# Kernel optimization log

Hardware: AMD Instinct MI355X
Metric: run time of the kernel (lower is better)

## Reference

```python
import jax, jax.numpy as jnp
import numpy as np

B, T, C, H, O = 256, 256, 32, 512, 32
OUT_TIME = 32


def setup_inputs() -> dict:
    key = jax.random.key(0)
    ks = jax.random.split(key, 10)
    times = jnp.arange(T, dtype=jnp.float32)
    coeffs = jax.random.normal(ks[0], (B, T, C), jnp.float32)
    final_index = jax.random.randint(ks[1], (B,), 0, T)
    dW = jax.random.normal(ks[2], (T - 1, B, H), jnp.float32)  # unit-normal; scaled by sqrt(dt) inside
    s = lambda k, shape, fan: jax.random.normal(k, shape, jnp.float32) / np.float32(np.sqrt(fan))
    return {
        "times": times, "coeffs": coeffs, "final_index": final_index, "dW": dW,
        "W_init": s(ks[3], (C, H), C), "b_init": jnp.zeros((H,), jnp.float32),
        "W1": s(ks[4], (H + C, H), H + C), "b1": jnp.zeros((H,), jnp.float32),
        "W2": s(ks[5], (H, H), H), "b2": jnp.zeros((H,), jnp.float32),
        "Wg": s(ks[6], (H, H), H), "bg": jnp.zeros((H,), jnp.float32),
        "Wh1": s(ks[7], (H, H), H), "bh1": jnp.zeros((H,), jnp.float32),
        "Wh2": s(ks[8], (H, O), H), "bh2": jnp.zeros((O,), jnp.float32),
    }


def reference(times, coeffs, final_index, dW, W_init, b_init, W1, b1, W2, b2, Wg, bg, Wh1, bh1, Wh2, bh2):
    # dt = max(min(diff(times)), 0.001)  (Euler method default in the torch module)
    dt = jnp.maximum(jnp.min(times[1:] - times[:-1]), jnp.float32(0.001))
    sqdt = jnp.sqrt(dt)

    x_seq = jnp.transpose(coeffs, (1, 0, 2))  # [T, B, C] control path at grid points
    # z0 = initial_network(X.evaluate(times[0]))
    z0 = x_seq[0] @ W_init + b_init  # [B, H]

    def step(y, inp):
        xk, dWk = inp  # [B, C], [B, H]
        h = jnp.tanh(jnp.concatenate([y, xk], axis=-1) @ W1 + b1)
        f = jnp.tanh(h @ W2 + b2)                # drift
        g = jax.nn.sigmoid(y @ Wg + bg)          # diagonal diffusion
        y_next = y + f * dt + g * (sqdt * dWk)   # Euler-Maruyama step
        return y_next, y_next

    _, zs = jax.lax.scan(step, z0, (x_seq[:-1], dW))  # zs: [T-1, B, H]
    z = jnp.concatenate([z0[None], zs], axis=0)       # [T, B, H]
    z = jnp.transpose(z, (1, 0, 2))                   # [B, T, H]  (transpose loop in torch code)
    z_tail = z[:, z.shape[1] - OUT_TIME:, :]          # last output_time steps
    return jax.nn.relu(z_tail @ Wh1 + bh1) @ Wh2 + bh2  # [B, OUT_TIME, O]
```

## Files before the change

### kernel.cpp

```cpp
#include <hip/hip_runtime.h>
#include <stdint.h>
#include <stddef.h>

typedef __attribute__((ext_vector_type(8))) short short8;
typedef __attribute__((ext_vector_type(8))) _Float16 half8;
typedef __attribute__((ext_vector_type(4))) float f32x4;
typedef unsigned long long ull;

#define T_  256
#define B_  256
#define C_  32
#define H_  512
#define O_  32
#define KB1 17
#define NT1 64
#define KB2 16
#define NT2 32

__device__ __forceinline__ short f2h(float f) {
  _Float16 h = (_Float16)f;
  return __builtin_bit_cast(short, h);
}
__device__ __forceinline__ void f2hl(float f, short& hi, short& lo) {
  _Float16 h = (_Float16)f;
  _Float16 l = (_Float16)(f - (float)h);
  hi = __builtin_bit_cast(short, h);
  lo = __builtin_bit_cast(short, l);
}
__device__ __forceinline__ unsigned int pack_hl(float f) {
  short h, l;
  f2hl(f, h, l);
  return (unsigned int)(unsigned short)h | ((unsigned int)(unsigned short)l << 16);
}
__device__ __forceinline__ float fast_tanh(float x) {
  float e = __expf(2.0f * x);
  return 1.0f - 2.0f / (e + 1.0f);
}
__device__ __forceinline__ float fast_sigmoid(float x) {
  return 1.0f / (1.0f + __expf(-x));
}
__device__ __forceinline__ f32x4 mfma16(half8 a, half8 b, f32x4 c) {
  return __builtin_amdgcn_mfma_f32_16x16x32_f16(a, b, c, 0, 0, 0);
}
__device__ __forceinline__ half8 ld8(const short* p) { return *(const half8*)p; }

__device__ __forceinline__ void st_coh(unsigned int* p, unsigned int v) {
  __hip_atomic_store(p, v, __ATOMIC_RELAXED, __HIP_MEMORY_SCOPE_AGENT);
}
__device__ __forceinline__ ull ld_coh(const ull* p) {
  return __hip_atomic_load(p, __ATOMIC_RELAXED, __HIP_MEMORY_SCOPE_AGENT);
}

__device__ __forceinline__ void stage_pl(const ull* src, short* hi, short* lo,
                                         int stride, int tid) {
  ull v[16];
  #pragma unroll
  for (int i = 0; i < 8; ++i) {
    int p = i * 256 + tid;
    v[2 * i]     = ld_coh(src + 2 * p);
    v[2 * i + 1] = ld_coh(src + 2 * p + 1);
  }
  #pragma unroll
  for (int i = 0; i < 8; ++i) {
    int p = i * 256 + tid;
    int row = p >> 7, col4 = (p & 127) << 2;
    unsigned int u0 = (unsigned int)v[2 * i],     u1 = (unsigned int)(v[2 * i] >> 32);
    unsigned int u2 = (unsigned int)v[2 * i + 1], u3 = (unsigned int)(v[2 * i + 1] >> 32);
    unsigned int hiA = (u0 & 0xffffu) | (u1 << 16);
    unsigned int hiB = (u2 & 0xffffu) | (u3 << 16);
    unsigned int loA = (u0 >> 16) | (u1 & 0xffff0000u);
    unsigned int loB = (u2 >> 16) | (u3 & 0xffff0000u);
    *(ull*)(hi + row * stride + col4) = (ull)hiA | ((ull)hiB << 32);
    *(ull*)(lo + row * stride + col4) = (ull)loA | ((ull)loB << 32);
  }
}

__device__ __forceinline__ void bg_barrier(unsigned int* cnt, unsigned int target) {
  __syncthreads();
  if (threadIdx.x == 0) {
    __hip_atomic_fetch_add(cnt, 1u, __ATOMIC_RELAXED, __HIP_MEMORY_SCOPE_AGENT);
    while (__hip_atomic_load(cnt, __ATOMIC_RELAXED, __HIP_MEMORY_SCOPE_AGENT) < target)
      __builtin_amdgcn_s_sleep(1);
  }
  __syncthreads();
}

__global__ void pack_b1s(const float* __restrict__ W1, const float* __restrict__ Wg,
                         short* __restrict__ hi, short* __restrict__ lo) {
  int gid = blockIdx.x * 256 + threadIdx.x;
  if (gid >= KB1 * NT1 * 512) return;
  int j = gid & 7, lane = (gid >> 3) & 63, tile = gid >> 9;
  int nt = tile % NT1, kb = tile / NT1;
  int k = kb * 32 + ((lane >> 4) << 3) + j;
  int n = ((nt & 31) << 4) + (lane & 15);
  float v = 0.f;
  if (nt < 32)      v = W1[k * H_ + n];
  else if (k < H_)  v = Wg[k * H_ + n];
  short h, l;
  f2hl(v, h, l);
  hi[gid] = h; lo[gid] = l;
}

__global__ void pack_s(const float* __restrict__ src, short* __restrict__ hi,
                       short* __restrict__ lo, int Ksrc, int Nsrc, int KB, int NT) {
  int gid = blockIdx.x * 256 + threadIdx.x;
  if (gid >= KB * NT * 512) return;
  int j = gid & 7, lane = (gid >> 3) & 63, tile = gid >> 9;
  int nt = tile % NT, kb = tile / NT;
  int k = kb * 32 + ((lane >> 4) << 3) + j;
  int n = (nt << 4) + (lane & 15);
  float v = (k < Ksrc && n < Nsrc) ? src[k * Nsrc + n] : 0.f;
  short h, l;
  f2hl(v, h, l);
  hi[gid] = h;
  if (lo) lo[gid] = l;
}

__global__ __launch_bounds__(256, 1) void sde_kernel(
    const float* __restrict__ times, const float* __restrict__ coeffs,
    const float* __restrict__ dW,
    const float* __restrict__ b_init, const float* __restrict__ b1,
    const float* __restrict__ b2, const float* __restrict__ bgb,
    const short* __restrict__ B1h, const short* __restrict__ B1l,
    const short* __restrict__ W2h, const short* __restrict__ W2l,
    const short* __restrict__ WIh, const short* __restrict__ WIl,
    unsigned int* __restrict__ y_pk, unsigned int* __restrict__ h_pk,
    short* __restrict__ zt, unsigned int* __restrict__ cnt_base) {
  __shared__ short yx_hi[16][552];
  __shared__ short yx_lo[16][552];
  __shared__ short hh_hi[16][520];
  __shared__ short hh_lo[16][520];
  __shared__ float g_x[16][32];
  __shared__ float redbuf[4];

  const int tid = threadIdx.x;
  const int w = tid >> 6, l = tid & 63;
  const int ra = l & 15, kq = l >> 4;
  const int bid = blockIdx.x;
  const int bg = bid & 15, cg = bid >> 4;
  const int R0 = bg << 4;
  unsigned int* cnt = cnt_base + bg * 32;

  const int nt1w = (w < 2) ? (2 * cg + w) : (32 + 2 * cg + (w - 2));
  const int extcol = nt1w * 16 + ra;
  const int ntF = 2 * cg + (w & 1);
  const int fcol = ntF * 16 + ra;

  float d = 1e30f;
  if (tid < T_ - 1) d = times[tid + 1] - times[tid];
  #pragma unroll
  for (int s = 32; s >= 1; s >>= 1) d = fminf(d, __shfl_xor(d, s, 64));
  if (l == 0) redbuf[w] = d;

  half8 wb1h[17], wb1l[17];
  #pragma unroll
  for (int kb = 0; kb < 17; ++kb) {
    const size_t off = ((size_t)(kb * 64 + nt1w) << 9) + (l << 3);
    wb1h[kb] = ld8(B1h + off);
    wb1l[kb] = ld8(B1l + off);
  }
  half8 ww2h[16], ww2l[16];
  if (w < 2) {
    #pragma unroll
    for (int kb = 0; kb < 16; ++kb) {
      const size_t off = ((size_t)(kb * 32 + ntF) << 9) + (l << 3);
      ww2h[kb] = ld8(W2h + off);
      ww2l[kb] = ld8(W2l + off);
    }
  }

  if (tid < 64) {
    int row = tid >> 2, cc = (tid & 3) << 3;
    const float* xb = coeffs + (size_t)(R0 + row) * (T_ * C_) + cc;
    short8 hi, lo;
    #pragma unroll
    for (int j = 0; j < 8; ++j) {
      short h, l2;
      f2hl(xb[j], h, l2);
      hi[j] = h; lo[j] = l2;
    }
    *(short8*)&yx_hi[row][512 + cc] = hi;
    *(short8*)&yx_lo[row][512 + cc] = lo;
  }
  __syncthreads();
  float m = fminf(fminf(redbuf[0], redbuf[1]), fminf(redbuf[2], redbuf[3]));
  const float dt = fmaxf(m, 0.001f);
  const float sq = sqrtf(dt);

  const float b1v = (w < 2) ? b1[extcol] : 0.f;
  const float bgv = (w >= 2) ? bgb[extcol - 512] : 0.f;
  const float b2v = (w < 2) ? b2[fcol] : 0.f;

  float yr[4] = {0.f, 0.f, 0.f, 0.f};
  if (w < 2) {
    half8 ah = ld8(&yx_hi[ra][512 + (kq << 3)]);
    half8 al = ld8(&yx_lo[ra][512 + (kq << 3)]);
    half8 bh = ld8(WIh + ((size_t)ntF << 9) + (l << 3));
    half8 bl = ld8(WIl + ((size_t)ntF << 9) + (l << 3));
    f32x4 Z = {0.f, 0.f, 0.f, 0.f};
    Z = mfma16(ah, bh, Z); Z = mfma16(al, bh, Z); Z = mfma16(ah, bl, Z);
    float bi = b_init[fcol];
    #pragma unroll
    for (int r = 0; r < 4; ++r) {
      yr[r] = Z[r] + bi;
      st_coh(&y_pk[(size_t)(R0 + (kq << 2) + r) * H_ + fcol], pack_hl(yr[r]));
    }
  }
  bg_barrier(cnt, 16u);

  for (int k = 0; k < T_ - 1; ++k) {
    float dwv[4];
    if (w < 2) {
      const float* dwb = dW + ((size_t)k * B_ + R0) * H_ + fcol;
      #pragma unroll
      for (int r = 0; r < 4; ++r)
        dwv[r] = __builtin_nontemporal_load(dwb + ((kq << 2) + r) * H_);
    }
    stage_pl((const ull*)y_pk + R0 * 256, &yx_hi[0][0], &yx_lo[0][0], 552, tid);
    __syncthreads();
    f32x4 Aa = {0.f, 0.f, 0.f, 0.f}, Ab = Aa, Ac = Aa;
    #pragma unroll
    for (int kb = 0; kb < 17; ++kb) {
      half8 ah = ld8(&yx_hi[ra][(kb << 5) + (kq << 3)]);
      half8 al = ld8(&yx_lo[ra][(kb << 5) + (kq << 3)]);
      Aa = mfma16(ah, wb1h[kb], Aa);
      Ab = mfma16(al, wb1h[kb], Ab);
      Ac = mfma16(ah, wb1l[kb], Ac);
    }
    if (w < 2) {
      #pragma unroll
      for (int r = 0; r < 4; ++r) {
        float h = fast_tanh((Aa[r] + Ab[r]) + Ac[r] + b1v);
        st_coh(&h_pk[(size_t)(R0 + (kq << 2) + r) * H_ + extcol], pack_hl(h));
      }
    } else {
      #pragma unroll
      for (int r = 0; r < 4; ++r)
        g_x[(kq << 2) + r][((w - 2) << 4) + ra] =
            fast_sigmoid((Aa[r] + Ab[r]) + Ac[r] + bgv);
    }
    bg_barrier(cnt, 16u * (2u * (unsigned)k + 2u));
    stage_pl((const ull*)h_pk + R0 * 256, &hh_hi[0][0], &hh_lo[0][0], 520, tid);
    __syncthreads();
    if (w < 2) {
      f32x4 Fa = {0.f, 0.f, 0.f, 0.f}, Fb = Fa, Fc = Fa;
      #pragma unroll
      for (int kb = 0; kb < 16; ++kb) {
        half8 ah = ld8(&hh_hi[ra][(kb << 5) + (kq << 3)]);
        half8 al = ld8(&hh_lo[ra][(kb << 5) + (kq << 3)]);
        Fa = mfma16(ah, ww2h[kb], Fa);
        Fb = mfma16(al, ww2h[kb], Fb);
        Fc = mfma16(ah, ww2l[kb], Fc);
      }
      #pragma unroll
      for (int r = 0; r < 4; ++r) {
        float f = fast_tanh((Fa[r] + Fb[r]) + Fc[r] + b2v);
        float g = g_x[(kq << 2) + r][((w & 1) << 4) + ra];
        yr[r] += f * dt + g * (sq * dwv[r]);
        st_coh(&y_pk[(size_t)(R0 + (kq << 2) + r) * H_ + fcol], pack_hl(yr[r]));
      }
      if (k >= T_ - 1 - O_) {
        int t = k - (T_ - 1 - O_);
        #pragma unroll
        for (int r = 0; r < 4; ++r)
          zt[((size_t)(R0 + (kq << 2) + r) * O_ + t) * H_ + fcol] = f2h(yr[r]);
      }
    } else if (w == 2 && k < T_ - 2) {
      int row = l >> 2, cc = (l & 3) << 3;
      const float* xb =
          coeffs + (size_t)(R0 + row) * (T_ * C_) + (size_t)(k + 1) * C_ + cc;
      short8 hi, lo;
      #pragma unroll
      for (int j = 0; j < 8; ++j) {
        short h, l2;
        f2hl(xb[j], h, l2);
        hi[j] = h; lo[j] = l2;
      }
      *(short8*)&yx_hi[row][512 + cc] = hi;
      *(short8*)&yx_lo[row][512 + cc] = lo;
    }
    bg_barrier(cnt, 16u * (2u * (unsigned)k + 3u));
  }
}

__global__ __launch_bounds__(256) void head_kernel(
    const short* __restrict__ zt, const short* __restrict__ Wh1p,
    const short* __restrict__ Wh2p, const float* __restrict__ bh1,
    const float* __restrict__ bh2, float* __restrict__ out) {
  __shared__ short a_lds[32][520];
  __shared__ short h2_lds[32][520];
  const int tid = threadIdx.x;
  const int w = tid >> 6, l = tid & 63;
  const int ra = l & 15, kq = l >> 4;
  const int r0 = blockIdx.x << 5;

  const short* zb = zt + (size_t)r0 * H_;
  #pragma unroll
  for (int i = 0; i < 8; ++i) {
    int cidx = i * 256 + tid;
    int row = cidx >> 6, cc = (cidx & 63) << 3;
    *(short8*)&a_lds[row][cc] = *(const short8*)(zb + row * H_ + cc);
  }
  __syncthreads();

  f32x4 acc[2][8];
  #pragma unroll
  for (int mt = 0; mt < 2; ++mt)
    #pragma unroll
    for (int i = 0; i < 8; ++i) acc[mt][i] = (f32x4){0.f, 0.f, 0.f, 0.f};
  for (int kb = 0; kb < 16; ++kb) {
    half8 a0 = ld8(&a_lds[ra][(kb << 5) + (kq << 3)]);
    half8 a1 = ld8(&a_lds[16 + ra][(kb << 5) + (kq << 3)]);
    const short* bp = Wh1p + (size_t)kb * (32 * 512) + (l << 3);
    #pragma unroll
    for (int i = 0; i < 8; ++i) {
      half8 b = ld8(bp + ((8 * w + i) << 9));
      acc[0][i] = mfma16(a0, b, acc[0][i]);
      acc[1][i] = mfma16(a1, b, acc[1][i]);
    }
  }
  #pragma unroll
  for (int i = 0; i < 8; ++i) {
    int col = ((8 * w + i) << 4) + ra;
    float bb = bh1[col];
    #pragma unroll
    for (int mt = 0; mt < 2; ++mt)
      #pragma unroll
      for (int r = 0; r < 4; ++r) {
        float h = acc[mt][i][r] + bb;
        h = h > 0.f ? h : 0.f;
        h2_lds[(mt << 4) + (kq << 2) + r][col] = f2h(h);
      }
  }
  __syncthreads();

  {
    int mt = w >> 1, nt = w & 1;
    f32x4 F = {0.f, 0.f, 0.f, 0.f};
    for (int kb = 0; kb < 16; ++kb) {
      half8 a = ld8(&h2_lds[(mt << 4) + ra][(kb << 5) + (kq << 3)]);
      half8 b = ld8(Wh2p + (size_t)((kb * 2 + nt) * 64 + l) * 8);
      F = mfma16(a, b, F);
    }
    int col = (nt << 4) + ra;
    float bb = bh2[col];
    #pragma unroll
    for (int r = 0; r < 4; ++r)
      out[(size_t)(r0 + (mt << 4) + (kq << 2) + r) * O_ + col] = F[r] + bb;
  }
}

extern "C" void kernel_launch(void* const* d_in, const int* in_sizes, int n_in,
                              void* d_out, int out_size, void* d_ws, size_t ws_size,
                              hipStream_t stream) {
  (void)in_sizes; (void)n_in; (void)out_size; (void)ws_size;
  const float* times  = (const float*)d_in[0];
  const float* coeffs = (const float*)d_in[1];
  const float* dW     = (const float*)d_in[3];
  const float* W_init = (const float*)d_in[4];
  const float* b_init = (const float*)d_in[5];
  const float* W1     = (const float*)d_in[6];
  const float* b1     = (const float*)d_in[7];
  const float* W2     = (const float*)d_in[8];
  const float* b2     = (const float*)d_in[9];
  const float* Wg     = (const float*)d_in[10];
  const float* bg     = (const float*)d_in[11];
  const float* Wh1    = (const float*)d_in[12];
  const float* bh1    = (const float*)d_in[13];
  const float* Wh2    = (const float*)d_in[14];
  const float* bh2    = (const float*)d_in[15];
  float* out = (float*)d_out;
  char* ws = (char*)d_ws;

  short* B1h  = (short*)(ws + 0);
  short* B1l  = (short*)(ws + 1114112);
  short* W2h  = (short*)(ws + 2228224);
  short* W2l  = (short*)(ws + 2752512);
  short* WIh  = (short*)(ws + 3276800);
  short* WIl  = (short*)(ws + 3309568);
  short* Wh1p = (short*)(ws + 3342336);
  short* Wh2p = (short*)(ws + 3866624);
  unsigned int* y_pk = (unsigned int*)(ws + 3899392);
  unsigned int* h_pk = (unsigned int*)(ws + 4423680);
  short* zt   = (short*)(ws + 4947968);
  unsigned int* cnt = (unsigned int*)(ws + 13336576);

  pack_b1s<<<2176, 256, 0, stream>>>(W1, Wg, B1h, B1l);
  pack_s  <<<1024, 256, 0, stream>>>(W2, W2h, W2l, 512, 512, 16, 32);
  pack_s  <<<64,   256, 0, stream>>>(W_init, WIh, WIl, 32, 512, 1, 32);
  pack_s  <<<1024, 256, 0, stream>>>(Wh1, Wh1p, (short*)nullptr, 512, 512, 16, 32);
  pack_s  <<<64,   256, 0, stream>>>(Wh2, Wh2p, (short*)nullptr, 512, 32, 16, 2);

  hipMemsetAsync(ws + 13336576, 0, 2048, stream);

  sde_kernel<<<256, 256, 0, stream>>>(times, coeffs, dW, b_init, b1, b2, bg,
                                      B1h, B1l, W2h, W2l, WIh, WIl,
                                      y_pk, h_pk, zt, cnt);
  head_kernel<<<256, 256, 0, stream>>>(zt, Wh1p, Wh2p, bh1, bh2, out);
}
```

Before: 1.511 ms.

## Use 512-thread blocks and per-block flag barriers in the SDE loop

Halves the grid to 128 blocks of 512 threads, so each block computes four column tiles instead of two and each batch group has 8 cooperating blocks instead of 16. The shared atomic-counter barrier becomes per-block monotonic flags: each block publishes its step counter, and every wave polls the group's eight flags before staging shared state. This is meant to cut inter-block synchronisation latency and atomic contention on each of the two per-step barriers. In exchange, launch_bounds(512,2) tightens the per-thread register budget while the kernel keeps large register-resident weight fragments, which risks spilling.

Measured after the change: 2.839 ms. 87.9% more time.

```diff
diff --git a/kernel.cpp b/kernel.cpp
--- a/kernel.cpp
+++ b/kernel.cpp
@@ -47,22 +47,25 @@
 __device__ __forceinline__ void st_coh(unsigned int* p, unsigned int v) {
   __hip_atomic_store(p, v, __ATOMIC_RELAXED, __HIP_MEMORY_SCOPE_AGENT);
 }
+__device__ __forceinline__ unsigned int ld_cohu(const unsigned int* p) {
+  return __hip_atomic_load(p, __ATOMIC_RELAXED, __HIP_MEMORY_SCOPE_AGENT);
+}
 __device__ __forceinline__ ull ld_coh(const ull* p) {
   return __hip_atomic_load(p, __ATOMIC_RELAXED, __HIP_MEMORY_SCOPE_AGENT);
 }
 
 __device__ __forceinline__ void stage_pl(const ull* src, short* hi, short* lo,
                                          int stride, int tid) {
-  ull v[16];
-  #pragma unroll
-  for (int i = 0; i < 8; ++i) {
-    int p = i * 256 + tid;
+  ull v[8];
+  #pragma unroll
+  for (int i = 0; i < 4; ++i) {
+    int p = i * 512 + tid;
     v[2 * i]     = ld_coh(src + 2 * p);
     v[2 * i + 1] = ld_coh(src + 2 * p + 1);
   }
   #pragma unroll
-  for (int i = 0; i < 8; ++i) {
-    int p = i * 256 + tid;
+  for (int i = 0; i < 4; ++i) {
+    int p = i * 512 + tid;
     int row = p >> 7, col4 = (p & 127) << 2;
     unsigned int u0 = (unsigned int)v[2 * i],     u1 = (unsigned int)(v[2 * i] >> 32);
     unsigned int u2 = (unsigned int)v[2 * i + 1], u3 = (unsigned int)(v[2 * i + 1] >> 32);
@@ -75,14 +78,13 @@
   }
 }
 
-__device__ __forceinline__ void bg_barrier(unsigned int* cnt, unsigned int target) {
-  __syncthreads();
-  if (threadIdx.x == 0) {
-    __hip_atomic_fetch_add(cnt, 1u, __ATOMIC_RELAXED, __HIP_MEMORY_SCOPE_AGENT);
-    while (__hip_atomic_load(cnt, __ATOMIC_RELAXED, __HIP_MEMORY_SCOPE_AGENT) < target)
-      __builtin_amdgcn_s_sleep(1);
-  }
-  __syncthreads();
+__device__ __forceinline__ void bg_wait(const unsigned int* fl, unsigned int target) {
+  const int l = threadIdx.x & 63;
+  for (;;) {
+    unsigned int f = (l < 8) ? ld_cohu(fl + l * 32) : 0xffffffffu;
+    if (__all((l < 8) ? (f >= target) : 1)) break;
+  }
+  __builtin_amdgcn_sched_barrier(0);
 }
 
 __global__ void pack_b1s(const float* __restrict__ W1, const float* __restrict__ Wg,
@@ -116,7 +118,7 @@
   if (lo) lo[gid] = l;
 }
 
-__global__ __launch_bounds__(256, 1) void sde_kernel(
+__global__ __launch_bounds__(512, 2) void sde_kernel(
     const float* __restrict__ times, const float* __restrict__ coeffs,
     const float* __restrict__ dW,
     const float* __restrict__ b_init, const float* __restrict__ b1,
@@ -125,12 +127,12 @@
     const short* __restrict__ W2h, const short* __restrict__ W2l,
     const short* __restrict__ WIh, const short* __restrict__ WIl,
     unsigned int* __restrict__ y_pk, unsigned int* __restrict__ h_pk,
-    short* __restrict__ zt, unsigned int* __restrict__ cnt_base) {
+    short* __restrict__ zt, unsigned int* __restrict__ flags_base) {
   __shared__ short yx_hi[16][552];
   __shared__ short yx_lo[16][552];
   __shared__ short hh_hi[16][520];
   __shared__ short hh_lo[16][520];
-  __shared__ float g_x[16][32];
+  __shared__ float g_x[16][64];
   __shared__ float redbuf[4];
 
   const int tid = threadIdx.x;
@@ -139,18 +141,19 @@
   const int bid = blockIdx.x;
   const int bg = bid & 15, cg = bid >> 4;
   const int R0 = bg << 4;
-  unsigned int* cnt = cnt_base + bg * 32;
-
-  const int nt1w = (w < 2) ? (2 * cg + w) : (32 + 2 * cg + (w - 2));
+  unsigned int* flags = flags_base + (bg << 3) * 32;
+  unsigned int* myflag = flags + cg * 32;
+
+  const int nt1w = (w < 4) ? (4 * cg + w) : (32 + 4 * cg + (w - 4));
   const int extcol = nt1w * 16 + ra;
-  const int ntF = 2 * cg + (w & 1);
+  const int ntF = 4 * cg + (w & 3);
   const int fcol = ntF * 16 + ra;
 
   float d = 1e30f;
   if (tid < T_ - 1) d = times[tid + 1] - times[tid];
   #pragma unroll
   for (int s = 32; s >= 1; s >>= 1) d = fminf(d, __shfl_xor(d, s, 64));
-  if (l == 0) redbuf[w] = d;
+  if (w < 4 && l == 0) redbuf[w] = d;
 
   half8 wb1h[17], wb1l[17];
   #pragma unroll
@@ -160,7 +163,7 @@
     wb1l[kb] = ld8(B1l + off);
   }
   half8 ww2h[16], ww2l[16];
-  if (w < 2) {
+  if (w < 4) {
     #pragma unroll
     for (int kb = 0; kb < 16; ++kb) {
       const size_t off = ((size_t)(kb * 32 + ntF) << 9) + (l << 3);
@@ -187,12 +190,12 @@
   const float dt = fmaxf(m, 0.001f);
   const float sq = sqrtf(dt);
 
-  const float b1v = (w < 2) ? b1[extcol] : 0.f;
-  const float bgv = (w >= 2) ? bgb[extcol - 512] : 0.f;
-  const float b2v = (w < 2) ? b2[fcol] : 0.f;
+  const float b1v = (w < 4) ? b1[extcol] : 0.f;
+  const float bgv = (w >= 4) ? bgb[extcol - 512] : 0.f;
+  const float b2v = (w < 4) ? b2[fcol] : 0.f;
 
   float yr[4] = {0.f, 0.f, 0.f, 0.f};
-  if (w < 2) {
+  if (w < 4) {
     half8 ah = ld8(&yx_hi[ra][512 + (kq << 3)]);
     half8 al = ld8(&yx_lo[ra][512 + (kq << 3)]);
     half8 bh = ld8(WIh + ((size_t)ntF << 9) + (l << 3));
@@ -206,16 +209,18 @@
       st_coh(&y_pk[(size_t)(R0 + (kq << 2) + r) * H_ + fcol], pack_hl(yr[r]));
     }
   }
-  bg_barrier(cnt, 16u);
+  __syncthreads();
+  if (tid == 0) st_coh(myflag, 1u);
 
   for (int k = 0; k < T_ - 1; ++k) {
     float dwv[4];
-    if (w < 2) {
+    if (w < 4) {
       const float* dwb = dW + ((size_t)k * B_ + R0) * H_ + fcol;
       #pragma unroll
       for (int r = 0; r < 4; ++r)
         dwv[r] = __builtin_nontemporal_load(dwb + ((kq << 2) + r) * H_);
     }
+    bg_wait(flags, 2u * (unsigned)k + 1u);
     stage_pl((const ull*)y_pk + R0 * 256, &yx_hi[0][0], &yx_lo[0][0], 552, tid);
     __syncthreads();
     f32x4 Aa = {0.f, 0.f, 0.f, 0.f}, Ab = Aa, Ac = Aa;
@@ -227,7 +232,7 @@
       Ab = mfma16(al, wb1h[kb], Ab);
       Ac = mfma16(ah, wb1l[kb], Ac);
     }
-    if (w < 2) {
+    if (w < 4) {
       #pragma unroll
       for (int r = 0; r < 4; ++r) {
         float h = fast_tanh((Aa[r] + Ab[r]) + Ac[r] + b1v);
@@ -236,13 +241,16 @@
     } else {
       #pragma unroll
       for (int r = 0; r < 4; ++r)
-        g_x[(kq << 2) + r][((w - 2) << 4) + ra] =
+        g_x[(kq << 2) + r][((w - 4) << 4) + ra] =
             fast_sigmoid((Aa[r] + Ab[r]) + Ac[r] + bgv);
     }
-    bg_barrier(cnt, 16u * (2u * (unsigned)k + 2u));
+    __syncthreads();
+    if (tid == 0) st_coh(myflag, 2u * (unsigned)k + 2u);
+
+    bg_wait(flags, 2u * (unsigned)k + 2u);
     stage_pl((const ull*)h_pk + R0 * 256, &hh_hi[0][0], &hh_lo[0][0], 520, tid);
     __syncthreads();
-    if (w < 2) {
+    if (w < 4) {
       f32x4 Fa = {0.f, 0.f, 0.f, 0.f}, Fb = Fa, Fc = Fa;
       #pragma unroll
       for (int kb = 0; kb < 16; ++kb) {
@@ -255,7 +263,7 @@
       #pragma unroll
       for (int r = 0; r < 4; ++r) {
         float f = fast_tanh((Fa[r] + Fb[r]) + Fc[r] + b2v);
-        float g = g_x[(kq << 2) + r][((w & 1) << 4) + ra];
+        float g = g_x[(kq << 2) + r][((w & 3) << 4) + ra];
         yr[r] += f * dt + g * (sq * dwv[r]);
         st_coh(&y_pk[(size_t)(R0 + (kq << 2) + r) * H_ + fcol], pack_hl(yr[r]));
       }
@@ -265,7 +273,7 @@
         for (int r = 0; r < 4; ++r)
           zt[((size_t)(R0 + (kq << 2) + r) * O_ + t) * H_ + fcol] = f2h(yr[r]);
       }
-    } else if (w == 2 && k < T_ - 2) {
+    } else if (w == 4 && k < T_ - 2) {
       int row = l >> 2, cc = (l & 3) << 3;
       const float* xb =
           coeffs + (size_t)(R0 + row) * (T_ * C_) + (size_t)(k + 1) * C_ + cc;
@@ -279,7 +287,8 @@
       *(short8*)&yx_hi[row][512 + cc] = hi;
       *(short8*)&yx_lo[row][512 + cc] = lo;
     }
-    bg_barrier(cnt, 16u * (2u * (unsigned)k + 3u));
+    __syncthreads();
+    if (tid == 0) st_coh(myflag, 2u * (unsigned)k + 3u);
   }
 }
 
@@ -383,7 +392,7 @@
   unsigned int* y_pk = (unsigned int*)(ws + 3899392);
   unsigned int* h_pk = (unsigned int*)(ws + 4423680);
   short* zt   = (short*)(ws + 4947968);
-  unsigned int* cnt = (unsigned int*)(ws + 13336576);
+  unsigned int* flags = (unsigned int*)(ws + 13336576);
 
   pack_b1s<<<2176, 256, 0, stream>>>(W1, Wg, B1h, B1l);
   pack_s  <<<1024, 256, 0, stream>>>(W2, W2h, W2l, 512, 512, 16, 32);
@@ -391,10 +400,10 @@
   pack_s  <<<1024, 256, 0, stream>>>(Wh1, Wh1p, (short*)nullptr, 512, 512, 16, 32);
   pack_s  <<<64,   256, 0, stream>>>(Wh2, Wh2p, (short*)nullptr, 512, 32, 16, 2);
 
-  hipMemsetAsync(ws + 13336576, 0, 2048, stream);
-
-  sde_kernel<<<256, 256, 0, stream>>>(times, coeffs, dW, b_init, b1, b2, bg,
+  hipMemsetAsync(ws + 13336576, 0, 16384, stream);
+
+  sde_kernel<<<128, 512, 0, stream>>>(times, coeffs, dW, b_init, b1, b2, bg,
                                       B1h, B1l, W2h, W2l, WIh, WIl,
-                                      y_pk, h_pk, zt, cnt);
+                                      y_pk, h_pk, zt, flags);
   head_kernel<<<256, 256, 0, stream>>>(zt, Wh1p, Wh2p, bh1, bh2, out);
 }
```

## Replace atomic counter barrier with per-block flags and split arrive/wait

Applied to the files above, without the earlier changes.

Swaps the shared atomic-increment barrier for per-block monotonic flags. Each block publishes its phase with a relaxed store after a local sync, and waits by having one wavefront poll all 16 peer flags in parallel until every flag reaches the target. This removes atomic contention on one counter and the second __syncthreads, and moves the dW load ahead of the wait so it overlaps. Relaxed atomics without explicit fences carry a memory-ordering risk, and every wavefront now spin-polls without sleeping, which can add memory traffic.

Result: slower. 1.735 ms (+14.8%).

```diff
diff --git a/kernel.cpp b/kernel.cpp
--- a/kernel.cpp
+++ b/kernel.cpp
@@ -46,6 +46,9 @@
 
 __device__ __forceinline__ void st_coh(unsigned int* p, unsigned int v) {
   __hip_atomic_store(p, v, __ATOMIC_RELAXED, __HIP_MEMORY_SCOPE_AGENT);
+}
+__device__ __forceinline__ unsigned int ld_cohu(const unsigned int* p) {
+  return __hip_atomic_load(p, __ATOMIC_RELAXED, __HIP_MEMORY_SCOPE_AGENT);
 }
 __device__ __forceinline__ ull ld_coh(const ull* p) {
   return __hip_atomic_load(p, __ATOMIC_RELAXED, __HIP_MEMORY_SCOPE_AGENT);
@@ -75,14 +78,13 @@
   }
 }
 
-__device__ __forceinline__ void bg_barrier(unsigned int* cnt, unsigned int target) {
-  __syncthreads();
-  if (threadIdx.x == 0) {
-    __hip_atomic_fetch_add(cnt, 1u, __ATOMIC_RELAXED, __HIP_MEMORY_SCOPE_AGENT);
-    while (__hip_atomic_load(cnt, __ATOMIC_RELAXED, __HIP_MEMORY_SCOPE_AGENT) < target)
-      __builtin_amdgcn_s_sleep(1);
-  }
-  __syncthreads();
+__device__ __forceinline__ void bg_wait(const unsigned int* fl, unsigned int target) {
+  const int l = threadIdx.x & 63;
+  for (;;) {
+    unsigned int f = (l < 16) ? ld_cohu(fl + l * 32) : 0xffffffffu;
+    if (__all((l < 16) ? (f >= target) : 1)) break;
+  }
+  __builtin_amdgcn_sched_barrier(0);
 }
 
 __global__ void pack_b1s(const float* __restrict__ W1, const float* __restrict__ Wg,
@@ -125,7 +127,7 @@
     const short* __restrict__ W2h, const short* __restrict__ W2l,
     const short* __restrict__ WIh, const short* __restrict__ WIl,
     unsigned int* __restrict__ y_pk, unsigned int* __restrict__ h_pk,
-    short* __restrict__ zt, unsigned int* __restrict__ cnt_base) {
+    short* __restrict__ zt, unsigned int* __restrict__ flags_base) {
   __shared__ short yx_hi[16][552];
   __shared__ short yx_lo[16][552];
   __shared__ short hh_hi[16][520];
@@ -139,7 +141,8 @@
   const int bid = blockIdx.x;
   const int bg = bid & 15, cg = bid >> 4;
   const int R0 = bg << 4;
-  unsigned int* cnt = cnt_base + bg * 32;
+  unsigned int* flags = flags_base + (bg << 4) * 32;
+  unsigned int* myflag = flags + cg * 32;
 
   const int nt1w = (w < 2) ? (2 * cg + w) : (32 + 2 * cg + (w - 2));
   const int extcol = nt1w * 16 + ra;
@@ -206,7 +209,8 @@
       st_coh(&y_pk[(size_t)(R0 + (kq << 2) + r) * H_ + fcol], pack_hl(yr[r]));
     }
   }
-  bg_barrier(cnt, 16u);
+  __syncthreads();
+  if (tid == 0) st_coh(myflag, 1u);
 
   for (int k = 0; k < T_ - 1; ++k) {
     float dwv[4];
@@ -216,6 +220,7 @@
       for (int r = 0; r < 4; ++r)
         dwv[r] = __builtin_nontemporal_load(dwb + ((kq << 2) + r) * H_);
     }
+    bg_wait(flags, 2u * (unsigned)k + 1u);
     stage_pl((const ull*)y_pk + R0 * 256, &yx_hi[0][0], &yx_lo[0][0], 552, tid);
     __syncthreads();
     f32x4 Aa = {0.f, 0.f, 0.f, 0.f}, Ab = Aa, Ac = Aa;
@@ -239,7 +244,10 @@
         g_x[(kq << 2) + r][((w - 2) << 4) + ra] =
             fast_sigmoid((Aa[r] + Ab[r]) + Ac[r] + bgv);
     }
-    bg_barrier(cnt, 16u * (2u * (unsigned)k + 2u));
+    __syncthreads();
+    if (tid == 0) st_coh(myflag, 2u * (unsigned)k + 2u);
+
+    bg_wait(flags, 2u * (unsigned)k + 2u);
     stage_pl((const ull*)h_pk + R0 * 256, &hh_hi[0][0], &hh_lo[0][0], 520, tid);
     __syncthreads();
     if (w < 2) {
@@ -279,7 +287,8 @@
       *(short8*)&yx_hi[row][512 + cc] = hi;
       *(short8*)&yx_lo[row][512 + cc] = lo;
     }
-    bg_barrier(cnt, 16u * (2u * (unsigned)k + 3u));
+    __syncthreads();
+    if (tid == 0) st_coh(myflag, 2u * (unsigned)k + 3u);
   }
 }
 
@@ -383,7 +392,7 @@
   unsigned int* y_pk = (unsigned int*)(ws + 3899392);
   unsigned int* h_pk = (unsigned int*)(ws + 4423680);
   short* zt   = (short*)(ws + 4947968);
-  unsigned int* cnt = (unsigned int*)(ws + 13336576);
+  unsigned int* flags = (unsigned int*)(ws + 13336576);
 
   pack_b1s<<<2176, 256, 0, stream>>>(W1, Wg, B1h, B1l);
   pack_s  <<<1024, 256, 0, stream>>>(W2, W2h, W2l, 512, 512, 16, 32);
@@ -391,10 +400,10 @@
   pack_s  <<<1024, 256, 0, stream>>>(Wh1, Wh1p, (short*)nullptr, 512, 512, 16, 32);
   pack_s  <<<64,   256, 0, stream>>>(Wh2, Wh2p, (short*)nullptr, 512, 32, 16, 2);
 
-  hipMemsetAsync(ws + 13336576, 0, 2048, stream);
+  hipMemsetAsync(ws + 13336576, 0, 32768, stream);
 
   sde_kernel<<<256, 256, 0, stream>>>(times, coeffs, dW, b_init, b1, b2, bg,
                                       B1h, B1l, W2h, W2l, WIh, WIl,
-                                      y_pk, h_pk, zt, cnt);
+                                      y_pk, h_pk, zt, flags);
   head_kernel<<<256, 256, 0, stream>>>(zt, Wh1p, Wh2p, bh1, bh2, out);
 }
```

## Split each block's batch rows into two independent 8-row groups to overlap barrier waits

Applied to the files above, without the earlier changes.

Each block now serves two independent 8-row batch groups (A and B), each with its own cross-block counter. The blocking barrier is split into separate signal and wait steps, so one group's compute can run while the other group's barrier latency is pending. The cost is that the 16x16 MFMA tiles are only half used (8 valid rows), roughly doubling MFMA issue per useful row, and the group counters need twice the memset space.

Measured after the change: 2.206 ms. 46.0% more time.

```diff
diff --git a/kernel.cpp b/kernel.cpp
--- a/kernel.cpp
+++ b/kernel.cpp
@@ -3,6 +3,7 @@
 #include <stddef.h>
 
 typedef __attribute__((ext_vector_type(8))) short short8;
+typedef __attribute__((ext_vector_type(4))) short short4v;
 typedef __attribute__((ext_vector_type(8))) _Float16 half8;
 typedef __attribute__((ext_vector_type(4))) float f32x4;
 typedef unsigned long long ull;
@@ -51,38 +52,41 @@
   return __hip_atomic_load(p, __ATOMIC_RELAXED, __HIP_MEMORY_SCOPE_AGENT);
 }
 
-__device__ __forceinline__ void stage_pl(const ull* src, short* hi, short* lo,
-                                         int stride, int tid) {
-  ull v[16];
-  #pragma unroll
-  for (int i = 0; i < 8; ++i) {
-    int p = i * 256 + tid;
-    v[2 * i]     = ld_coh(src + 2 * p);
-    v[2 * i + 1] = ld_coh(src + 2 * p + 1);
-  }
-  #pragma unroll
-  for (int i = 0; i < 8; ++i) {
-    int p = i * 256 + tid;
-    int row = p >> 7, col4 = (p & 127) << 2;
+__device__ __forceinline__ void sig(unsigned int* cnt) {
+  __syncthreads();
+  if (threadIdx.x == 0)
+    __hip_atomic_fetch_add(cnt, 1u, __ATOMIC_RELAXED, __HIP_MEMORY_SCOPE_AGENT);
+}
+__device__ __forceinline__ void wt(unsigned int* cnt, unsigned int target) {
+  if (threadIdx.x == 0) {
+    while (__hip_atomic_load(cnt, __ATOMIC_RELAXED, __HIP_MEMORY_SCOPE_AGENT) < target)
+      __builtin_amdgcn_s_sleep(1);
+  }
+  __syncthreads();
+}
+
+__device__ __forceinline__ void stage8(const ull* src, short* hi, short* lo,
+                                       int stride, int tid) {
+  ull v[8];
+  #pragma unroll
+  for (int i = 0; i < 4; ++i) {
+    int u = i * 512 + 2 * tid;
+    v[2 * i]     = ld_coh(src + u);
+    v[2 * i + 1] = ld_coh(src + u + 1);
+  }
+  #pragma unroll
+  for (int i = 0; i < 4; ++i) {
+    int u = i * 512 + 2 * tid;
+    int row = u >> 8, c = (u & 255) * 2;
     unsigned int u0 = (unsigned int)v[2 * i],     u1 = (unsigned int)(v[2 * i] >> 32);
     unsigned int u2 = (unsigned int)v[2 * i + 1], u3 = (unsigned int)(v[2 * i + 1] >> 32);
     unsigned int hiA = (u0 & 0xffffu) | (u1 << 16);
     unsigned int hiB = (u2 & 0xffffu) | (u3 << 16);
     unsigned int loA = (u0 >> 16) | (u1 & 0xffff0000u);
     unsigned int loB = (u2 >> 16) | (u3 & 0xffff0000u);
-    *(ull*)(hi + row * stride + col4) = (ull)hiA | ((ull)hiB << 32);
-    *(ull*)(lo + row * stride + col4) = (ull)loA | ((ull)loB << 32);
-  }
-}
-
-__device__ __forceinline__ void bg_barrier(unsigned int* cnt, unsigned int target) {
-  __syncthreads();
-  if (threadIdx.x == 0) {
-    __hip_atomic_fetch_add(cnt, 1u, __ATOMIC_RELAXED, __HIP_MEMORY_SCOPE_AGENT);
-    while (__hip_atomic_load(cnt, __ATOMIC_RELAXED, __HIP_MEMORY_SCOPE_AGENT) < target)
-      __builtin_amdgcn_s_sleep(1);
-  }
-  __syncthreads();
+    *(ull*)(hi + row * stride + c) = (ull)hiA | ((ull)hiB << 32);
+    *(ull*)(lo + row * stride + c) = (ull)loA | ((ull)loB << 32);
+  }
 }
 
 __global__ void pack_b1s(const float* __restrict__ W1, const float* __restrict__ Wg,
@@ -126,25 +130,27 @@
     const short* __restrict__ WIh, const short* __restrict__ WIl,
     unsigned int* __restrict__ y_pk, unsigned int* __restrict__ h_pk,
     short* __restrict__ zt, unsigned int* __restrict__ cnt_base) {
-  __shared__ short yx_hi[16][552];
-  __shared__ short yx_lo[16][552];
-  __shared__ short hh_hi[16][520];
-  __shared__ short hh_lo[16][520];
-  __shared__ float g_x[16][32];
+  __shared__ short yxA_hi[8][552], yxA_lo[8][552];
+  __shared__ short yxB_hi[8][552], yxB_lo[8][552];
+  __shared__ short hhA_hi[8][520], hhA_lo[8][520];
+  __shared__ short hhB_hi[8][520], hhB_lo[8][520];
+  __shared__ float gA[8][32], gB[8][32];
   __shared__ float redbuf[4];
 
   const int tid = threadIdx.x;
   const int w = tid >> 6, l = tid & 63;
   const int ra = l & 15, kq = l >> 4;
   const int bid = blockIdx.x;
-  const int bg = bid & 15, cg = bid >> 4;
-  const int R0 = bg << 4;
-  unsigned int* cnt = cnt_base + bg * 32;
+  const int pair = bid & 15, cg = bid >> 4;
+  const int R0A = pair << 3, R0B = (pair + 16) << 3;
+  unsigned int* cntA = cnt_base + pair * 32;
+  unsigned int* cntB = cnt_base + (pair + 16) * 32;
 
   const int nt1w = (w < 2) ? (2 * cg + w) : (32 + 2 * cg + (w - 2));
   const int extcol = nt1w * 16 + ra;
   const int ntF = 2 * cg + (w & 1);
   const int fcol = ntF * 16 + ra;
+  const int ra8 = ra & 7;
 
   float d = 1e30f;
   if (tid < T_ - 1) d = times[tid + 1] - times[tid];
@@ -169,18 +175,24 @@
     }
   }
 
-  if (tid < 64) {
-    int row = tid >> 2, cc = (tid & 3) << 3;
-    const float* xb = coeffs + (size_t)(R0 + row) * (T_ * C_) + cc;
-    short8 hi, lo;
+  if (w == 2 || w == 3) {
+    int row = l >> 3, c0 = (l & 7) << 2;
+    const float* xb =
+        coeffs + (size_t)(((w == 2) ? R0A : R0B) + row) * (T_ * C_) + c0;
+    short4v hi, lo;
     #pragma unroll
-    for (int j = 0; j < 8; ++j) {
+    for (int j = 0; j < 4; ++j) {
       short h, l2;
       f2hl(xb[j], h, l2);
       hi[j] = h; lo[j] = l2;
     }
-    *(short8*)&yx_hi[row][512 + cc] = hi;
-    *(short8*)&yx_lo[row][512 + cc] = lo;
+    if (w == 2) {
+      *(short4v*)&yxA_hi[row][512 + c0] = hi;
+      *(short4v*)&yxA_lo[row][512 + c0] = lo;
+    } else {
+      *(short4v*)&yxB_hi[row][512 + c0] = hi;
+      *(short4v*)&yxB_lo[row][512 + c0] = lo;
+    }
   }
   __syncthreads();
   float m = fminf(fminf(redbuf[0], redbuf[1]), fminf(redbuf[2], redbuf[3]));
@@ -191,95 +203,203 @@
   const float bgv = (w >= 2) ? bgb[extcol - 512] : 0.f;
   const float b2v = (w < 2) ? b2[fcol] : 0.f;
 
-  float yr[4] = {0.f, 0.f, 0.f, 0.f};
+  float yrA[4] = {0.f, 0.f, 0.f, 0.f}, yrB[4] = {0.f, 0.f, 0.f, 0.f};
   if (w < 2) {
-    half8 ah = ld8(&yx_hi[ra][512 + (kq << 3)]);
-    half8 al = ld8(&yx_lo[ra][512 + (kq << 3)]);
     half8 bh = ld8(WIh + ((size_t)ntF << 9) + (l << 3));
     half8 bl = ld8(WIl + ((size_t)ntF << 9) + (l << 3));
-    f32x4 Z = {0.f, 0.f, 0.f, 0.f};
-    Z = mfma16(ah, bh, Z); Z = mfma16(al, bh, Z); Z = mfma16(ah, bl, Z);
     float bi = b_init[fcol];
-    #pragma unroll
-    for (int r = 0; r < 4; ++r) {
-      yr[r] = Z[r] + bi;
-      st_coh(&y_pk[(size_t)(R0 + (kq << 2) + r) * H_ + fcol], pack_hl(yr[r]));
-    }
-  }
-  bg_barrier(cnt, 16u);
+    {
+      half8 ah = ld8(&yxA_hi[ra8][512 + (kq << 3)]);
+      half8 al = ld8(&yxA_lo[ra8][512 + (kq << 3)]);
+      f32x4 Z = {0.f, 0.f, 0.f, 0.f};
+      Z = mfma16(ah, bh, Z); Z = mfma16(al, bh, Z); Z = mfma16(ah, bl, Z);
+      if (kq < 2) {
+        #pragma unroll
+        for (int r = 0; r < 4; ++r) {
+          yrA[r] = Z[r] + bi;
+          st_coh(&y_pk[(size_t)(R0A + (kq << 2) + r) * H_ + fcol], pack_hl(yrA[r]));
+        }
+      }
+    }
+    {
+      half8 ah = ld8(&yxB_hi[ra8][512 + (kq << 3)]);
+      half8 al = ld8(&yxB_lo[ra8][512 + (kq << 3)]);
+      f32x4 Z = {0.f, 0.f, 0.f, 0.f};
+      Z = mfma16(ah, bh, Z); Z = mfma16(al, bh, Z); Z = mfma16(ah, bl, Z);
+      if (kq < 2) {
+        #pragma unroll
+        for (int r = 0; r < 4; ++r) {
+          yrB[r] = Z[r] + bi;
+          st_coh(&y_pk[(size_t)(R0B + (kq << 2) + r) * H_ + fcol], pack_hl(yrB[r]));
+        }
+      }
+    }
+  }
+  __syncthreads();
+  if (tid == 0) {
+    __hip_atomic_fetch_add(cntA, 1u, __ATOMIC_RELAXED, __HIP_MEMORY_SCOPE_AGENT);
+    __hip_atomic_fetch_add(cntB, 1u, __ATOMIC_RELAXED, __HIP_MEMORY_SCOPE_AGENT);
+  }
 
   for (int k = 0; k < T_ - 1; ++k) {
-    float dwv[4];
-    if (w < 2) {
-      const float* dwb = dW + ((size_t)k * B_ + R0) * H_ + fcol;
-      #pragma unroll
-      for (int r = 0; r < 4; ++r)
-        dwv[r] = __builtin_nontemporal_load(dwb + ((kq << 2) + r) * H_);
-    }
-    stage_pl((const ull*)y_pk + R0 * 256, &yx_hi[0][0], &yx_lo[0][0], 552, tid);
+    float dwA[4], dwB[4];
+    if (w < 2 && kq < 2) {
+      const float* dwbA = dW + ((size_t)k * B_ + R0A) * H_ + fcol;
+      const float* dwbB = dW + ((size_t)k * B_ + R0B) * H_ + fcol;
+      #pragma unroll
+      for (int r = 0; r < 4; ++r) {
+        dwA[r] = __builtin_nontemporal_load(dwbA + ((kq << 2) + r) * H_);
+        dwB[r] = __builtin_nontemporal_load(dwbB + ((kq << 2) + r) * H_);
+      }
+    }
+
+    wt(cntA, 16u * (2u * (unsigned)k + 1u));
+    stage8((const ull*)y_pk + R0A * 256, &yxA_hi[0][0], &yxA_lo[0][0], 552, tid);
     __syncthreads();
-    f32x4 Aa = {0.f, 0.f, 0.f, 0.f}, Ab = Aa, Ac = Aa;
-    #pragma unroll
-    for (int kb = 0; kb < 17; ++kb) {
-      half8 ah = ld8(&yx_hi[ra][(kb << 5) + (kq << 3)]);
-      half8 al = ld8(&yx_lo[ra][(kb << 5) + (kq << 3)]);
-      Aa = mfma16(ah, wb1h[kb], Aa);
-      Ab = mfma16(al, wb1h[kb], Ab);
-      Ac = mfma16(ah, wb1l[kb], Ac);
-    }
-    if (w < 2) {
-      #pragma unroll
-      for (int r = 0; r < 4; ++r) {
-        float h = fast_tanh((Aa[r] + Ab[r]) + Ac[r] + b1v);
-        st_coh(&h_pk[(size_t)(R0 + (kq << 2) + r) * H_ + extcol], pack_hl(h));
-      }
-    } else {
-      #pragma unroll
-      for (int r = 0; r < 4; ++r)
-        g_x[(kq << 2) + r][((w - 2) << 4) + ra] =
-            fast_sigmoid((Aa[r] + Ab[r]) + Ac[r] + bgv);
-    }
-    bg_barrier(cnt, 16u * (2u * (unsigned)k + 2u));
-    stage_pl((const ull*)h_pk + R0 * 256, &hh_hi[0][0], &hh_lo[0][0], 520, tid);
+    {
+      f32x4 Aa = {0.f, 0.f, 0.f, 0.f}, Ab = Aa, Ac = Aa;
+      #pragma unroll
+      for (int kb = 0; kb < 17; ++kb) {
+        half8 ah = ld8(&yxA_hi[ra8][(kb << 5) + (kq << 3)]);
+        half8 al = ld8(&yxA_lo[ra8][(kb << 5) + (kq << 3)]);
+        Aa = mfma16(ah, wb1h[kb], Aa);
+        Ab = mfma16(al, wb1h[kb], Ab);
+        Ac = mfma16(ah, wb1l[kb], Ac);
+      }
+      if (kq < 2) {
+        if (w < 2) {
+          #pragma unroll
+          for (int r = 0; r < 4; ++r) {
+            float h = fast_tanh((Aa[r] + Ab[r]) + Ac[r] + b1v);
+            st_coh(&h_pk[(size_t)(R0A + (kq << 2) + r) * H_ + extcol], pack_hl(h));
+          }
+        } else {
+          #pragma unroll
+          for (int r = 0; r < 4; ++r)
+            gA[(kq << 2) + r][((w - 2) << 4) + ra] =
+                fast_sigmoid((Aa[r] + Ab[r]) + Ac[r] + bgv);
+        }
+      }
+    }
+    sig(cntA);
+
+    wt(cntB, 16u * (2u * (unsigned)k + 1u));
+    stage8((const ull*)y_pk + R0B * 256, &yxB_hi[0][0], &yxB_lo[0][0], 552, tid);
+    __syncthreads();
+    {
+      f32x4 Aa = {0.f, 0.f, 0.f, 0.f}, Ab = Aa, Ac = Aa;
+      #pragma unroll
+      for (int kb = 0; kb < 17; ++kb) {
+        half8 ah = ld8(&yxB_hi[ra8][(kb << 5) + (kq << 3)]);
+        half8 al = ld8(&yxB_lo[ra8][(kb << 5) + (kq << 3)]);
+        Aa = mfma16(ah, wb1h[kb], Aa);
+        Ab = mfma16(al, wb1h[kb], Ab);
+        Ac = mfma16(ah, wb1l[kb], Ac);
+      }
+      if (kq < 2) {
+        if (w < 2) {
+          #pragma unroll
+          for (int r = 0; r < 4; ++r) {
+            float h = fast_tanh((Aa[r] + Ab[r]) + Ac[r] + b1v);
+            st_coh(&h_pk[(size_t)(R0B + (kq << 2) + r) * H_ + extcol], pack_hl(h));
+          }
+        } else {
+          #pragma unroll
+          for (int r = 0; r < 4; ++r)
+            gB[(kq << 2) + r][((w - 2) << 4) + ra] =
+                fast_sigmoid((Aa[r] + Ab[r]) + Ac[r] + bgv);
+        }
+      }
+    }
+    sig(cntB);
+
+    wt(cntA, 16u * (2u * (unsigned)k + 2u));
+    stage8((const ull*)h_pk + R0A * 256, &hhA_hi[0][0], &hhA_lo[0][0], 520, tid);
     __syncthreads();
     if (w < 2) {
       f32x4 Fa = {0.f, 0.f, 0.f, 0.f}, Fb = Fa, Fc = Fa;
       #pragma unroll
       for (int kb = 0; kb < 16; ++kb) {
-        half8 ah = ld8(&hh_hi[ra][(kb << 5) + (kq << 3)]);
-        half8 al = ld8(&hh_lo[ra][(kb << 5) + (kq << 3)]);
+        half8 ah = ld8(&hhA_hi[ra8][(kb << 5) + (kq << 3)]);
+        half8 al = ld8(&hhA_lo[ra8][(kb << 5) + (kq << 3)]);
         Fa = mfma16(ah, ww2h[kb], Fa);
         Fb = mfma16(al, ww2h[kb], Fb);
         Fc = mfma16(ah, ww2l[kb], Fc);
       }
-      #pragma unroll
-      for (int r = 0; r < 4; ++r) {
-        float f = fast_tanh((Fa[r] + Fb[r]) + Fc[r] + b2v);
-        float g = g_x[(kq << 2) + r][((w & 1) << 4) + ra];
-        yr[r] += f * dt + g * (sq * dwv[r]);
-        st_coh(&y_pk[(size_t)(R0 + (kq << 2) + r) * H_ + fcol], pack_hl(yr[r]));
-      }
-      if (k >= T_ - 1 - O_) {
-        int t = k - (T_ - 1 - O_);
+      if (kq < 2) {
         #pragma unroll
-        for (int r = 0; r < 4; ++r)
-          zt[((size_t)(R0 + (kq << 2) + r) * O_ + t) * H_ + fcol] = f2h(yr[r]);
+        for (int r = 0; r < 4; ++r) {
+          float f = fast_tanh((Fa[r] + Fb[r]) + Fc[r] + b2v);
+          float g = gA[(kq << 2) + r][((w & 1) << 4) + ra];
+          yrA[r] += f * dt + g * (sq * dwA[r]);
+          st_coh(&y_pk[(size_t)(R0A + (kq << 2) + r) * H_ + fcol], pack_hl(yrA[r]));
+        }
+        if (k >= T_ - 1 - O_) {
+          int t = k - (T_ - 1 - O_);
+          #pragma unroll
+          for (int r = 0; r < 4; ++r)
+            zt[((size_t)(R0A + (kq << 2) + r) * O_ + t) * H_ + fcol] = f2h(yrA[r]);
+        }
       }
     } else if (w == 2 && k < T_ - 2) {
-      int row = l >> 2, cc = (l & 3) << 3;
+      int row = l >> 3, c0 = (l & 7) << 2;
       const float* xb =
-          coeffs + (size_t)(R0 + row) * (T_ * C_) + (size_t)(k + 1) * C_ + cc;
-      short8 hi, lo;
-      #pragma unroll
-      for (int j = 0; j < 8; ++j) {
+          coeffs + (size_t)(R0A + row) * (T_ * C_) + (size_t)(k + 1) * C_ + c0;
+      short4v hi, lo;
+      #pragma unroll
+      for (int j = 0; j < 4; ++j) {
         short h, l2;
         f2hl(xb[j], h, l2);
         hi[j] = h; lo[j] = l2;
       }
-      *(short8*)&yx_hi[row][512 + cc] = hi;
-      *(short8*)&yx_lo[row][512 + cc] = lo;
-    }
-    bg_barrier(cnt, 16u * (2u * (unsigned)k + 3u));
+      *(short4v*)&yxA_hi[row][512 + c0] = hi;
+      *(short4v*)&yxA_lo[row][512 + c0] = lo;
+    }
+    sig(cntA);
+
+    wt(cntB, 16u * (2u * (unsigned)k + 2u));
+    stage8((const ull*)h_pk + R0B * 256, &hhB_hi[0][0], &hhB_lo[0][0], 520, tid);
+    __syncthreads();
+    if (w < 2) {
+      f32x4 Fa = {0.f, 0.f, 0.f, 0.f}, Fb = Fa, Fc = Fa;
+      #pragma unroll
+      for (int kb = 0; kb < 16; ++kb) {
+        half8 ah = ld8(&hhB_hi[ra8][(kb << 5) + (kq << 3)]);
+        half8 al = ld8(&hhB_lo[ra8][(kb << 5) + (kq << 3)]);
+        Fa = mfma16(ah, ww2h[kb], Fa);
+        Fb = mfma16(al, ww2h[kb], Fb);
+        Fc = mfma16(ah, ww2l[kb], Fc);
+      }
+      if (kq < 2) {
+        #pragma unroll
+        for (int r = 0; r < 4; ++r) {
+          float f = fast_tanh((Fa[r] + Fb[r]) + Fc[r] + b2v);
+          float g = gB[(kq << 2) + r][((w & 1) << 4) + ra];
+          yrB[r] += f * dt + g * (sq * dwB[r]);
+          st_coh(&y_pk[(size_t)(R0B + (kq << 2) + r) * H_ + fcol], pack_hl(yrB[r]));
+        }
+        if (k >= T_ - 1 - O_) {
+          int t = k - (T_ - 1 - O_);
+          #pragma unroll
+          for (int r = 0; r < 4; ++r)
+            zt[((size_t)(R0B + (kq << 2) + r) * O_ + t) * H_ + fcol] = f2h(yrB[r]);
+        }
+      }
+    } else if (w == 3 && k < T_ - 2) {
+      int row = l >> 3, c0 = (l & 7) << 2;
+      const float* xb =
+          coeffs + (size_t)(R0B + row) * (T_ * C_) + (size_t)(k + 1) * C_ + c0;
+      short4v hi, lo;
+      #pragma unroll
+      for (int j = 0; j < 4; ++j) {
+        short h, l2;
+        f2hl(xb[j], h, l2);
+        hi[j] = h; lo[j] = l2;
+      }
+      *(short4v*)&yxB_hi[row][512 + c0] = hi;
+      *(short4v*)&yxB_lo[row][512 + c0] = lo;
+    }
+    sig(cntB);
   }
 }
 
@@ -391,7 +511,7 @@
   pack_s  <<<1024, 256, 0, stream>>>(Wh1, Wh1p, (short*)nullptr, 512, 512, 16, 32);
   pack_s  <<<64,   256, 0, stream>>>(Wh2, Wh2p, (short*)nullptr, 512, 32, 16, 2);
 
-  hipMemsetAsync(ws + 13336576, 0, 2048, stream);
+  hipMemsetAsync(ws + 13336576, 0, 4096, stream);
 
   sde_kernel<<<256, 256, 0, stream>>>(times, coeffs, dW, b_init, b1, b2, bg,
                                       B1h, B1l, W2h, W2l, WIh, WIl,
```
